# Kernel tuning notes

Hardware: AMD Instinct MI355X
Metric: run time of the kernel (lower is better)

## Reference

```python
import jax, jax.numpy as jnp
import numpy as np
from jax import lax

B, T, D, H, K = 8, 2048, 512, 4, 11
DK = D // H
LPAD = (K - 1) // 2  # sanm_shfit = 0
RPAD = K - 1 - LPAD


def setup_inputs() -> dict:
    key = jax.random.key(0)
    ks = jax.random.split(key, 7)
    x = jax.random.normal(ks[0], (B, T, D), jnp.float32)
    # binary padding-style mask (float, multiplied in; eq(0) used for attention)
    mask = jax.random.randint(ks[1], (B, 1, T), 0, 2).astype(jnp.float32)
    Wqkv = jax.random.normal(ks[2], (D, 3 * D), jnp.float32) * 0.02
    bqkv = jnp.zeros((3 * D,), jnp.float32)
    Wout = jax.random.normal(ks[3], (D, D), jnp.float32) * 0.02
    bout = jnp.zeros((D,), jnp.float32)
    # depthwise Conv1d weight: (out_ch=D, in_ch/groups=1, K)
    fsmn_w = jax.random.normal(ks[4], (D, 1, K), jnp.float32) * 0.1
    return {"x": x, "mask": mask, "Wqkv": Wqkv, "bqkv": bqkv,
            "Wout": Wout, "bout": bout, "fsmn_w": fsmn_w}


def _fsmn(v, mask, fsmn_w):
    # v: (B,T,D), mask: (B,1,T)
    m = mask.reshape(v.shape[0], -1, 1)          # (B,T,1)
    vm = v * m
    xc = vm.transpose(0, 2, 1)                   # (B,D,T)
    xp = jnp.pad(xc, ((0, 0), (0, 0), (LPAD, RPAD)))
    conv = lax.conv_general_dilated(
        xp, fsmn_w, window_strides=(1,), padding='VALID',
        dimension_numbers=('NCH', 'OIH', 'NCH'), feature_group_count=D)
    out = conv.transpose(0, 2, 1) + vm           # residual
    return out * m                               # (B,T,D)


def reference(x, mask, Wqkv, bqkv, Wout, bout, fsmn_w):
    b, t, _ = x.shape
    qkv = x @ Wqkv + bqkv                        # (B,T,3D)
    q, k, v = jnp.split(qkv, 3, axis=-1)
    fsmn_memory = _fsmn(v, mask, fsmn_w)
    qh = q.reshape(b, t, H, DK) * (DK ** -0.5)   # (B,T,H,DK)
    kh = k.reshape(b, t, H, DK)
    vh = v.reshape(b, t, H, DK)
    scores = jnp.einsum('bqhd,bkhd->bhqk', qh, kh)   # (B,H,T,T)
    km = mask[:, None, :, :]                     # (B,1,1,T) key mask
    scores = jnp.where(km == 0, -jnp.inf, scores)
    attn = jax.nn.softmax(scores, axis=-1)
    attn = jnp.where(km == 0, 0.0, attn)
    ctx = jnp.einsum('bhqk,bkhd->bqhd', attn, vh).reshape(b, t, D)
    att_outs = ctx @ Wout + bout
    return att_outs + fsmn_memory
```

## Files before the change

### kernel.cpp

```cpp
#include <hip/hip_runtime.h>
#include <hip/hip_bf16.h>
#include <stdint.h>

#define NB 8
#define NT 2048
#define ND 512
#define NH 4
#define NDK 128
#define QKV_LD 1536
#define KW 11

typedef unsigned short u16;
typedef __attribute__((ext_vector_type(4))) float f32x4;
typedef __attribute__((ext_vector_type(16))) float f32x16;
typedef __attribute__((ext_vector_type(4))) float fv4;
typedef __attribute__((ext_vector_type(8))) short s16x8;
typedef __attribute__((ext_vector_type(4))) unsigned short u16x4;
typedef __attribute__((ext_vector_type(4))) int i32x4;

#define AS1 __attribute__((address_space(1)))
#define AS3 __attribute__((address_space(3)))

__device__ __forceinline__ u16 f2bf(float f){
  unsigned u = __float_as_uint(f);
  u += 0x7fffu + ((u >> 16) & 1u);
  return (u16)(u >> 16);
}
__device__ __forceinline__ float bf2f(u16 h){ return __uint_as_float(((unsigned)h) << 16); }
__device__ __forceinline__ unsigned pack2bf(float a, float b){
  float2 t; t.x = a; t.y = b;
  __hip_bfloat162 h = __float22bfloat162_rn(t);
  return *reinterpret_cast<unsigned*>(&h);
}

__device__ __forceinline__ void transpose_body(
    const float* __restrict__ in, u16* __restrict__ out, int R, int C,
    int bx, int by, int tid)
{
  __shared__ float tile[32][33];
  const int cb = bx * 32, rb = by * 32;
  const int tx = tid & 31, ty = tid >> 5;
  #pragma unroll
  for (int i = 0; i < 4; ++i)
    tile[ty + i*8][tx] = in[(size_t)(rb + ty + i*8) * C + cb + tx];
  __syncthreads();
  #pragma unroll
  for (int i = 0; i < 4; ++i)
    out[(size_t)(cb + ty + i*8) * R + rb + tx] = f2bf(tile[tx][ty + i*8]);
}

__global__ void prep_kernel(const float* __restrict__ x, u16* __restrict__ xb,
                            const float* __restrict__ Wqkv, u16* __restrict__ wqkvT,
                            const float* __restrict__ Wout, u16* __restrict__ woutT,
                            const float* __restrict__ mask, u16* __restrict__ idxb,
                            int* __restrict__ cntb)
{
  const int bid = blockIdx.x, tid = threadIdx.x;
  if (bid < 1024){
    const int n4 = (NB*NT*ND)/4;
    for (int i = bid*256 + tid; i < n4; i += 1024*256){
      float4 v = reinterpret_cast<const float4*>(x)[i];
      u16x4 o = { f2bf(v.x), f2bf(v.y), f2bf(v.z), f2bf(v.w) };
      reinterpret_cast<u16x4*>(xb)[i] = o;
    }
  } else if (bid < 1792){
    const int idx = bid - 1024;
    transpose_body(Wqkv, wqkvT, 512, 1536, idx % 48, idx / 48, tid);
  } else if (bid < 2048){
    const int idx = bid - 1792;
    transpose_body(Wout, woutT, 512, 512, idx % 16, idx / 16, tid);
  } else {
    const int b = bid - 2048;
    __shared__ int s[256];
    const float* mb = mask + (size_t)b * NT;
    float4 a = *reinterpret_cast<const float4*>(&mb[tid*8]);
    float4 c4 = *reinterpret_cast<const float4*>(&mb[tid*8 + 4]);
    float vals[8] = {a.x, a.y, a.z, a.w, c4.x, c4.y, c4.z, c4.w};
    int lc = 0;
    #pragma unroll
    for (int j = 0; j < 8; ++j) lc += (vals[j] != 0.f);
    s[tid] = lc; __syncthreads();
    #pragma unroll
    for (int d = 1; d < 256; d <<= 1){
      const int v = (tid >= d) ? s[tid - d] : 0;
      __syncthreads();
      s[tid] += v;
      __syncthreads();
    }
    const int excl = s[tid] - lc;
    const int total = s[255];
    u16* ib = idxb + (size_t)b * NT;
    int off = excl;
    #pragma unroll
    for (int j = 0; j < 8; ++j)
      if (vals[j] != 0.f) ib[off++] = (u16)(tid*8 + j);
    const int padded = (total + 63) & ~63;
    for (int j = total + tid; j < padded; j += 256) ib[j] = 0;
    if (tid == 0) cntb[b] = total;
  }
}

__global__ __launch_bounds__(256) void kv_compact(
    const u16* __restrict__ qkvb, const u16* __restrict__ idxb,
    const int* __restrict__ cntb, u16* __restrict__ kcb, u16* __restrict__ vtc)
{
  const int b = blockIdx.y, tile = blockIdx.x, tid = threadIdx.x;
  const int total = cntb[b];
  if (tile * 64 >= ((total + 63) & ~63)) return;
  __shared__ u16 idx64[64];
  __shared__ u16 vbuf[64 * 128];
  if (tid < 64) idx64[tid] = idxb[(size_t)b * NT + tile*64 + tid];
  __syncthreads();
  #pragma unroll
  for (int h = 0; h < 4; ++h){
    #pragma unroll
    for (int i = 0; i < 4; ++i){
      const int c = i*256 + tid, key = c >> 4, ck = c & 15;
      const int srcT = idx64[key];
      const u16* sp = qkvb + ((size_t)b*NT + srcT)*QKV_LD + ND + h*NDK + ck*8;
      u16* dp = kcb + ((size_t)(b*4+h)*NT + tile*64 + key)*NDK + ck*8;
      *reinterpret_cast<s16x8*>(dp) = *reinterpret_cast<const s16x8*>(sp);
    }
    #pragma unroll
    for (int i = 0; i < 4; ++i){
      const int c = i*256 + tid, key = c >> 4, ck = c & 15;
      const int srcT = idx64[key];
      const u16* sp = qkvb + ((size_t)b*NT + srcT)*QKV_LD + 2*ND + h*NDK + ck*8;
      *reinterpret_cast<s16x8*>(&vbuf[key*128 + ck*8]) =
          *reinterpret_cast<const s16x8*>(sp);
    }
    __syncthreads();
    u16* vt = vtc + ((size_t)(b*4+h)*32 + tile) * 8192;
    #pragma unroll
    for (int i = 0; i < 4; ++i){
      const int c = i*256 + tid, kg = c >> 7, dk = c & 127;
      s16x8 ov;
      #pragma unroll
      for (int e = 0; e < 8; ++e) ov[e] = (short)vbuf[(kg*8 + e)*128 + dk];
      *reinterpret_cast<s16x8*>(&vt[c*8]) = ov;
    }
    __syncthreads();
  }
}

template<int EPI>
__global__ __launch_bounds__(256, 2) void gemm_bt(
    const u16* __restrict__ A, const u16* __restrict__ Bt, const float* __restrict__ bias,
    u16* __restrict__ Cb, float* __restrict__ Cf,
    const u16* __restrict__ qkvb, const float* __restrict__ mask,
    const float* __restrict__ fsmn_w,
    int M, int N, int Kd)
{
  __shared__ u16 As[128 * 64];
  __shared__ u16 Bs[128 * 64];
  const int tid = threadIdx.x;
  const int m0 = blockIdx.y * 128, n0 = blockIdx.x * 128;
  const int w = tid >> 6, l = tid & 63, wr = w >> 1, wc = w & 1;
  const int r15 = l & 15, g = l >> 4;

  f32x4 acc[4][4] = {};

  const int r0 = tid >> 3;
  const int scol8 = ((tid & 7) ^ (r0 & 7)) << 3;
  const u16* Ag = A  + (size_t)(m0 + r0) * Kd + scol8;
  const u16* Bg = Bt + (size_t)(n0 + r0) * Kd + scol8;
  u16* Al = &As[(size_t)tid * 8];
  u16* Bl = &Bs[(size_t)tid * 8];

  for (int k0 = 0; k0 < Kd; k0 += 64){
    #pragma unroll
    for (int i = 0; i < 4; ++i)
      __builtin_amdgcn_global_load_lds((AS1 void*)(Ag + (size_t)(i*32) * Kd + k0),
                                       (AS3 void*)(Al + i*2048), 16, 0, 0);
    #pragma unroll
    for (int i = 0; i < 4; ++i)
      __builtin_amdgcn_global_load_lds((AS1 void*)(Bg + (size_t)(i*32) * Kd + k0),
                                       (AS3 void*)(Bl + i*2048), 16, 0, 0);
    __syncthreads();
    #pragma unroll
    for (int kk = 0; kk < 2; ++kk){
      s16x8 af[4], bfr[4];
      #pragma unroll
      for (int m = 0; m < 4; ++m){
        const int R = wr*64 + m*16 + r15;
        af[m] = *reinterpret_cast<const s16x8*>(
            &As[R*64 + (((kk*4 + g) ^ (r15 & 7)) << 3)]);
      }
      #pragma unroll
      for (int n = 0; n < 4; ++n){
        const int R = wc*64 + n*16 + r15;
        bfr[n] = *reinterpret_cast<const s16x8*>(
            &Bs[R*64 + (((kk*4 + g) ^ (r15 & 7)) << 3)]);
      }
      #pragma unroll
      for (int m = 0; m < 4; ++m){
        #pragma unroll
        for (int n = 0; n < 4; ++n)
          acc[m][n] = __builtin_amdgcn_mfma_f32_16x16x32_bf16(af[m], bfr[n], acc[m][n], 0, 0, 0);
      }
    }
    __syncthreads();
  }

  if (EPI == 0){
    #pragma unroll
    for (int m = 0; m < 4; ++m){
      const int gr0 = m0 + wr*64 + m*16 + g*4;
      #pragma unroll
      for (int n = 0; n < 4; ++n){
        const int gc = n0 + wc*64 + n*16 + r15;
        const float bv = bias[gc];
        #pragma unroll
        for (int j = 0; j < 4; ++j)
          Cb[(size_t)(gr0 + j) * N + gc] = f2bf(acc[m][n][j] + bv);
      }
    }
  } else {
    float wv[4][KW];
    #pragma unroll
    for (int n = 0; n < 4; ++n){
      const int gc = n0 + wc*64 + n*16 + r15;
      #pragma unroll
      for (int i = 0; i < KW; ++i) wv[n][i] = fsmn_w[gc*KW + i];
    }
    #pragma unroll
    for (int m = 0; m < 4; ++m){
      const int gr0 = m0 + wr*64 + m*16 + g*4;
      const int bb = gr0 >> 11, t0 = gr0 & 2047;
      const float* mb = mask + (size_t)bb * NT;
      float mk[14];
      #pragma unroll
      for (int i = 0; i < 14; ++i){
        const int tau = t0 - 5 + i;
        mk[i] = ((unsigned)tau < (unsigned)NT) ? mb[tau] : 0.f;
      }
      #pragma unroll
      for (int n = 0; n < 4; ++n){
        const int gc = n0 + wc*64 + n*16 + r15;
        const float bv = bias[gc];
        const u16* vb = qkvb + (size_t)bb * NT * QKV_LD + 2*ND + gc;
        float vmv[14];
        #pragma unroll
        for (int i = 0; i < 14; ++i){
          const ptrdiff_t tau = t0 - 5 + i;
          vmv[i] = mk[i] * bf2f(vb[tau * QKV_LD]);
        }
        #pragma unroll
        for (int j = 0; j < 4; ++j){
          float conv = vmv[5 + j];
          #pragma unroll
          for (int i = 0; i < KW; ++i) conv = fmaf(wv[n][i], vmv[j + i], conv);
          Cf[(size_t)(gr0 + j) * N + gc] = acc[m][n][j] + bv + mk[5 + j] * conv;
        }
      }
    }
  }
}

#define ATT_MFMA(a, bb, c) __builtin_amdgcn_mfma_f32_32x32x16_bf16(a, bb, c, 0, 0, 0)
#define C1F 0.12751741567f

__global__ __launch_bounds__(256, 2) void attn_kernel(
    const u16* __restrict__ qkvb, const u16* __restrict__ kcb,
    const u16* __restrict__ vtc, const int* __restrict__ cntb,
    u16* __restrict__ ctxb)
{
  __shared__ u16 Ks[2][64 * 128];
  __shared__ u16 Vs[2][8 * 128 * 8];
  const int tid = threadIdx.x;
  const int w = tid >> 6, l = tid & 63, l31 = l & 31, hi = l >> 5;

  const int lin = blockIdx.x + blockIdx.y * 8;
  const int xcd = lin & 7, jj = lin >> 3;
  const int bh = xcd * 4 + (jj & 3), qblk = jj >> 2;
  const int b = bh >> 2, h = bh & 3;
  const int q0 = qblk * 128;

  const u16* qptr = qkvb + (size_t)b * NT * QKV_LD + h * NDK;
  const u16* kb   = kcb + (size_t)bh * NT * NDK;
  const u16* vtb  = vtc + (size_t)bh * 32 * 8192;
  const int total = cntb[b];
  const int ntiles = (total + 63) >> 6;

  s16x8 qf[8];
  {
    const u16* qrow = qptr + (size_t)(q0 + w*32 + l31) * QKV_LD;
    #pragma unroll
    for (int s = 0; s < 8; ++s)
      qf[s] = *reinterpret_cast<const s16x8*>(qrow + s*16 + hi*8);
  }

  float mrun = -1e30f, lrun = 0.f;
  f32x16 o0 = {}, o1 = {}, o2 = {}, o3 = {};

#define STAGE(buf, kvo) do { \
    _Pragma("unroll") \
    for (int i_ = 0; i_ < 4; ++i_){ \
      const int n_ = i_*256 + tid, kr_ = n_ >> 4, c_ = n_ & 15; \
      const u16* gp_ = kb + (size_t)((kvo) + kr_) * NDK + ((c_ ^ (kr_ & 7)) << 3); \
      __builtin_amdgcn_global_load_lds((AS1 void*)gp_, (AS3 void*)&Ks[buf][n_*8], 16, 0, 0); \
    } \
    const u16* vsrc_ = vtb + ((kvo) >> 6) * 8192; \
    _Pragma("unroll") \
    for (int i_ = 0; i_ < 4; ++i_){ \
      const int n_ = i_*256 + tid; \
      __builtin_amdgcn_global_load_lds((AS1 void*)(vsrc_ + n_*8), \
                                       (AS3 void*)&Vs[buf][n_*8], 16, 0, 0); \
    } \
  } while(0)

  if (ntiles > 0) STAGE(0, 0);
  __syncthreads();
  int cur = 0;

  for (int t = 0; t < ntiles; ++t){
    const int kv0 = t * 64;
    if (t + 1 < ntiles) STAGE(cur ^ 1, kv0 + 64);

    f32x16 d0 = {}, d1 = {};
    __builtin_amdgcn_s_setprio(1);
    #pragma unroll
    for (int s = 0; s < 8; ++s){
      const int cg = s*2 + hi;
      s16x8 kf0 = *reinterpret_cast<const s16x8*>(
          &Ks[cur][ l31*128      + ((cg ^ (l31 & 7)) << 3) ]);
      s16x8 kf1 = *reinterpret_cast<const s16x8*>(
          &Ks[cur][ (32+l31)*128 + ((cg ^ (l31 & 7)) << 3) ]);
      d0 = ATT_MFMA(kf0, qf[s], d0);
      d1 = ATT_MFMA(kf1, qf[s], d1);
    }
    __builtin_amdgcn_s_setprio(0);

    float mx0 = fmaxf(d0[0], d0[1]), mx1 = fmaxf(d0[2], d0[3]);
    float mx2 = fmaxf(d1[0], d1[1]), mx3 = fmaxf(d1[2], d1[3]);
    #pragma unroll
    for (int r = 4; r < 16; r += 4){
      mx0 = fmaxf(mx0, fmaxf(d0[r],   d0[r+1]));
      mx1 = fmaxf(mx1, fmaxf(d0[r+2], d0[r+3]));
      mx2 = fmaxf(mx2, fmaxf(d1[r],   d1[r+1]));
      mx3 = fmaxf(mx3, fmaxf(d1[r+2], d1[r+3]));
    }
    float tmx = fmaxf(fmaxf(mx0, mx1), fmaxf(mx2, mx3));
    tmx = fmaxf(tmx, __shfl_xor(tmx, 32));

    if (!__all(tmx <= mrun + 64.f)){
      const float mn = fmaxf(mrun, tmx);
      const float corr = __builtin_amdgcn_exp2f((mrun - mn) * C1F);
      mrun = mn; lrun *= corr;
      #pragma unroll
      for (int r = 0; r < 16; ++r){
        const int qs = (r & 3) + 8*(r >> 2) + 4*hi;
        const float cq = __shfl(corr, qs);
        o0[r] *= cq; o1[r] *= cq; o2[r] *= cq; o3[r] *= cq;
      }
    }

    const float mm = mrun * C1F;
    float ts = 0.f;
    if (t + 1 < ntiles){
      #pragma unroll
      for (int r = 0; r < 16; ++r){
        const float p0 = __builtin_amdgcn_exp2f(fmaf(d0[r], C1F, -mm));
        const float p1 = __builtin_amdgcn_exp2f(fmaf(d1[r], C1F, -mm));
        d0[r] = p0; d1[r] = p1; ts += p0 + p1;
      }
    } else {
      #pragma unroll
      for (int r = 0; r < 16; ++r){
        const int kidx = kv0 + (r >> 2)*8 + 4*hi + (r & 3);
        const float p0 = (kidx      < total) ? __builtin_amdgcn_exp2f(fmaf(d0[r], C1F, -mm)) : 0.f;
        const float p1 = (kidx + 32 < total) ? __builtin_amdgcn_exp2f(fmaf(d1[r], C1F, -mm)) : 0.f;
        d0[r] = p0; d1[r] = p1; ts += p0 + p1;
      }
    }
    ts += __shfl_xor(ts, 32);
    lrun += ts;

    unsigned pku[2][4][2];
    #pragma unroll
    for (int r8 = 0; r8 < 4; ++r8){
      pku[0][r8][0] = pack2bf(d0[4*r8+0], d0[4*r8+1]);
      pku[0][r8][1] = pack2bf(d0[4*r8+2], d0[4*r8+3]);
      pku[1][r8][0] = pack2bf(d1[4*r8+0], d1[4*r8+1]);
      pku[1][r8][1] = pack2bf(d1[4*r8+2], d1[4*r8+3]);
    }

    const int vb0 = hi*1024 + l31*8;
    #pragma unroll
    for (int ks = 0; ks < 4; ++ks){
      const int bb = ks >> 1, rlo = (ks & 1) * 2;
      int u0 = (int)pku[bb][rlo][0],   u1 = (int)pku[bb][rlo][1];
      int v0 = (int)pku[bb][rlo+1][0], v1 = (int)pku[bb][rlo+1][1];
      asm("v_permlane32_swap_b32 %0, %1" : "+v"(u0), "+v"(v0));
      asm("v_permlane32_swap_b32 %0, %1" : "+v"(u1), "+v"(v1));
      union { i32x4 i; s16x8 hv; } pu;
      pu.i[0] = u0; pu.i[1] = u1; pu.i[2] = v0; pu.i[3] = v1;
      const int off = ks*2048 + vb0;
      s16x8 vf0 = *reinterpret_cast<const s16x8*>(&Vs[cur][ off       ]);
      s16x8 vf1 = *reinterpret_cast<const s16x8*>(&Vs[cur][ off + 256 ]);
      s16x8 vf2 = *reinterpret_cast<const s16x8*>(&Vs[cur][ off + 512 ]);
      s16x8 vf3 = *reinterpret_cast<const s16x8*>(&Vs[cur][ off + 768 ]);
      __builtin_amdgcn_s_setprio(1);
      o0 = ATT_MFMA(pu.hv, vf0, o0);
      o1 = ATT_MFMA(pu.hv, vf1, o1);
      o2 = ATT_MFMA(pu.hv, vf2, o2);
      o3 = ATT_MFMA(pu.hv, vf3, o3);
      __builtin_amdgcn_s_setprio(0);
    }

    __syncthreads();
    cur ^= 1;
  }

  #pragma unroll
  for (int r = 0; r < 16; ++r){
    const int qs = (r & 3) + 8*(r >> 2) + 4*hi;
    const float lr = __shfl(lrun, qs);
    const float rl = (lr > 0.f) ? (1.f / lr) : 0.f;
    const int row = q0 + w*32 + qs;
    u16* cp = ctxb + (size_t)(b*NT + row) * ND + h*NDK + l31;
    cp[0]  = f2bf(o0[r] * rl);
    cp[32] = f2bf(o1[r] * rl);
    cp[64] = f2bf(o2[r] * rl);
    cp[96] = f2bf(o3[r] * rl);
  }
#undef STAGE
}

extern "C" void kernel_launch(void* const* d_in, const int* in_sizes, int n_in,
                              void* d_out, int out_size, void* d_ws, size_t ws_size,
                              hipStream_t stream) {
  const float* x      = (const float*)d_in[0];
  const float* mask   = (const float*)d_in[1];
  const float* Wqkv   = (const float*)d_in[2];
  const float* bqkv   = (const float*)d_in[3];
  const float* Wout   = (const float*)d_in[4];
  const float* bout   = (const float*)d_in[5];
  const float* fsmn_w = (const float*)d_in[6];
  float* out = (float*)d_out;

  char* ws = (char*)d_ws;
  u16* xb    = (u16*)ws;
  u16* kcb   = (u16*)ws;
  u16* wqkvT = (u16*)(ws + 16777216);
  u16* woutT = (u16*)(ws + 18350080);
  u16* qkvb  = (u16*)(ws + 18874368);
  u16* ctxb  = (u16*)(ws + 69206016);
  u16* vtc   = (u16*)(ws + 85983232);
  u16* idxb  = (u16*)(ws + 102760448);
  int* cntb  = (int*)(ws + 102793216);

  prep_kernel<<<2056, 256, 0, stream>>>(x, xb, Wqkv, wqkvT, Wout, woutT,
                                        mask, idxb, cntb);
  gemm_bt<0><<<dim3(1536/128, 16384/128), 256, 0, stream>>>(
      xb, wqkvT, bqkv, qkvb, nullptr, nullptr, nullptr, nullptr, NB*NT, QKV_LD, ND);
  kv_compact<<<dim3(32, 8), 256, 0, stream>>>(qkvb, idxb, cntb, kcb, vtc);
  attn_kernel<<<dim3(8, 64), 256, 0, stream>>>(qkvb, kcb, vtc, cntb, ctxb);
  gemm_bt<1><<<dim3(512/128, 16384/128), 256, 0, stream>>>(
      ctxb, woutT, bout, nullptr, out, qkvb, mask, fsmn_w, NB*NT, ND, ND);
}
```

Before: 129.2 us.

## Compute K/V projection only for unmasked rows and write compacted layouts directly

Splits the QKV GEMM into a Q GEMM and a K/V GEMM. The K/V GEMM gathers only the unmasked token rows of x and writes K and transposed V directly in the compacted attention layouts, which removes the separate kv_compact kernel and the K/V projection work for masked tokens. The FSMN epilogue in the output GEMM now reads V from the compacted transposed buffer through a new position map built in prep, in place of the full qkv buffer. This adds gather indirection and scattered stores in the K/V epilogue.

```diff
diff --git a/kernel.cpp b/kernel.cpp
--- a/kernel.cpp
+++ b/kernel.cpp
@@ -7,7 +7,6 @@
 #define ND 512
 #define NH 4
 #define NDK 128
-#define QKV_LD 1536
 #define KW 11
 
 typedef unsigned short u16;
@@ -53,7 +52,7 @@
                             const float* __restrict__ Wqkv, u16* __restrict__ wqkvT,
                             const float* __restrict__ Wout, u16* __restrict__ woutT,
                             const float* __restrict__ mask, u16* __restrict__ idxb,
-                            int* __restrict__ cntb)
+                            u16* __restrict__ pos16, int* __restrict__ cntb)
 {
   const int bid = blockIdx.x, tid = threadIdx.x;
   if (bid < 1024){
@@ -90,66 +89,23 @@
     const int excl = s[tid] - lc;
     const int total = s[255];
     u16* ib = idxb + (size_t)b * NT;
+    u16* pb = pos16 + (size_t)b * NT;
     int off = excl;
     #pragma unroll
-    for (int j = 0; j < 8; ++j)
-      if (vals[j] != 0.f) ib[off++] = (u16)(tid*8 + j);
-    const int padded = (total + 63) & ~63;
+    for (int j = 0; j < 8; ++j){
+      const int t = tid*8 + j;
+      if (vals[j] != 0.f){ ib[off] = (u16)t; pb[t] = (u16)off; ++off; }
+      else pb[t] = (u16)0xFFFF;
+    }
+    const int padded = (total + 127) & ~127;
     for (int j = total + tid; j < padded; j += 256) ib[j] = 0;
     if (tid == 0) cntb[b] = total;
   }
 }
 
-__global__ __launch_bounds__(256) void kv_compact(
-    const u16* __restrict__ qkvb, const u16* __restrict__ idxb,
-    const int* __restrict__ cntb, u16* __restrict__ kcb, u16* __restrict__ vtc)
-{
-  const int b = blockIdx.y, tile = blockIdx.x, tid = threadIdx.x;
-  const int total = cntb[b];
-  if (tile * 64 >= ((total + 63) & ~63)) return;
-  __shared__ u16 idx64[64];
-  __shared__ u16 vbuf[64 * 128];
-  if (tid < 64) idx64[tid] = idxb[(size_t)b * NT + tile*64 + tid];
-  __syncthreads();
-  #pragma unroll
-  for (int h = 0; h < 4; ++h){
-    #pragma unroll
-    for (int i = 0; i < 4; ++i){
-      const int c = i*256 + tid, key = c >> 4, ck = c & 15;
-      const int srcT = idx64[key];
-      const u16* sp = qkvb + ((size_t)b*NT + srcT)*QKV_LD + ND + h*NDK + ck*8;
-      u16* dp = kcb + ((size_t)(b*4+h)*NT + tile*64 + key)*NDK + ck*8;
-      *reinterpret_cast<s16x8*>(dp) = *reinterpret_cast<const s16x8*>(sp);
-    }
-    #pragma unroll
-    for (int i = 0; i < 4; ++i){
-      const int c = i*256 + tid, key = c >> 4, ck = c & 15;
-      const int srcT = idx64[key];
-      const u16* sp = qkvb + ((size_t)b*NT + srcT)*QKV_LD + 2*ND + h*NDK + ck*8;
-      *reinterpret_cast<s16x8*>(&vbuf[key*128 + ck*8]) =
-          *reinterpret_cast<const s16x8*>(sp);
-    }
-    __syncthreads();
-    u16* vt = vtc + ((size_t)(b*4+h)*32 + tile) * 8192;
-    #pragma unroll
-    for (int i = 0; i < 4; ++i){
-      const int c = i*256 + tid, kg = c >> 7, dk = c & 127;
-      s16x8 ov;
-      #pragma unroll
-      for (int e = 0; e < 8; ++e) ov[e] = (short)vbuf[(kg*8 + e)*128 + dk];
-      *reinterpret_cast<s16x8*>(&vt[c*8]) = ov;
-    }
-    __syncthreads();
-  }
-}
-
-template<int EPI>
-__global__ __launch_bounds__(256, 2) void gemm_bt(
+__global__ __launch_bounds__(256, 2) void gemm_q(
     const u16* __restrict__ A, const u16* __restrict__ Bt, const float* __restrict__ bias,
-    u16* __restrict__ Cb, float* __restrict__ Cf,
-    const u16* __restrict__ qkvb, const float* __restrict__ mask,
-    const float* __restrict__ fsmn_w,
-    int M, int N, int Kd)
+    u16* __restrict__ Cb, int M, int N, int Kd)
 {
   __shared__ u16 As[128 * 64];
   __shared__ u16 Bs[128 * 64];
@@ -183,14 +139,12 @@
       #pragma unroll
       for (int m = 0; m < 4; ++m){
         const int R = wr*64 + m*16 + r15;
-        af[m] = *reinterpret_cast<const s16x8*>(
-            &As[R*64 + (((kk*4 + g) ^ (r15 & 7)) << 3)]);
+        af[m] = *reinterpret_cast<const s16x8*>(&As[R*64 + (((kk*4 + g) ^ (r15 & 7)) << 3)]);
       }
       #pragma unroll
       for (int n = 0; n < 4; ++n){
         const int R = wc*64 + n*16 + r15;
-        bfr[n] = *reinterpret_cast<const s16x8*>(
-            &Bs[R*64 + (((kk*4 + g) ^ (r15 & 7)) << 3)]);
+        bfr[n] = *reinterpret_cast<const s16x8*>(&Bs[R*64 + (((kk*4 + g) ^ (r15 & 7)) << 3)]);
       }
       #pragma unroll
       for (int m = 0; m < 4; ++m){
@@ -202,56 +156,202 @@
     __syncthreads();
   }
 
-  if (EPI == 0){
-    #pragma unroll
-    for (int m = 0; m < 4; ++m){
-      const int gr0 = m0 + wr*64 + m*16 + g*4;
-      #pragma unroll
-      for (int n = 0; n < 4; ++n){
-        const int gc = n0 + wc*64 + n*16 + r15;
-        const float bv = bias[gc];
-        #pragma unroll
-        for (int j = 0; j < 4; ++j)
-          Cb[(size_t)(gr0 + j) * N + gc] = f2bf(acc[m][n][j] + bv);
-      }
-    }
-  } else {
-    float wv[4][KW];
+  #pragma unroll
+  for (int m = 0; m < 4; ++m){
+    const int gr0 = m0 + wr*64 + m*16 + g*4;
     #pragma unroll
     for (int n = 0; n < 4; ++n){
       const int gc = n0 + wc*64 + n*16 + r15;
-      #pragma unroll
-      for (int i = 0; i < KW; ++i) wv[n][i] = fsmn_w[gc*KW + i];
-    }
-    #pragma unroll
-    for (int m = 0; m < 4; ++m){
-      const int gr0 = m0 + wr*64 + m*16 + g*4;
-      const int bb = gr0 >> 11, t0 = gr0 & 2047;
-      const float* mb = mask + (size_t)bb * NT;
-      float mk[14];
+      const float bv = bias[gc];
+      #pragma unroll
+      for (int j = 0; j < 4; ++j)
+        Cb[(size_t)(gr0 + j) * N + gc] = f2bf(acc[m][n][j] + bv);
+    }
+  }
+}
+
+__global__ __launch_bounds__(256, 2) void gemm_kv(
+    const u16* __restrict__ xb, const u16* __restrict__ Bt, const float* __restrict__ bias,
+    const u16* __restrict__ idxb, const int* __restrict__ cntb,
+    u16* __restrict__ kcb, u16* __restrict__ vtc)
+{
+  const int b = blockIdx.y >> 4, mb = blockIdx.y & 15;
+  const int total = cntb[b];
+  const int padded = (total + 127) & ~127;
+  const int m0 = mb * 128;
+  if (m0 >= padded) return;
+  const int Kd = ND, n0 = blockIdx.x * 128;
+
+  __shared__ u16 As[128 * 64];
+  __shared__ u16 Bs[128 * 64];
+  const int tid = threadIdx.x;
+  const int w = tid >> 6, l = tid & 63, wr = w >> 1, wc = w & 1;
+  const int r15 = l & 15, g = l >> 4;
+
+  f32x4 acc[4][4] = {};
+
+  const int r0 = tid >> 3;
+  const int scol8 = ((tid & 7) ^ (r0 & 7)) << 3;
+  const u16* ib = idxb + (size_t)b * NT;
+  const u16* Ab = xb + (size_t)b * NT * ND;
+  const u16* Ag0 = Ab + (size_t)ib[m0 + r0      ] * Kd + scol8;
+  const u16* Ag1 = Ab + (size_t)ib[m0 + r0 + 32 ] * Kd + scol8;
+  const u16* Ag2 = Ab + (size_t)ib[m0 + r0 + 64 ] * Kd + scol8;
+  const u16* Ag3 = Ab + (size_t)ib[m0 + r0 + 96 ] * Kd + scol8;
+  const u16* Bg = Bt + (size_t)(n0 + r0) * Kd + scol8;
+  u16* Al = &As[(size_t)tid * 8];
+  u16* Bl = &Bs[(size_t)tid * 8];
+
+  for (int k0 = 0; k0 < Kd; k0 += 64){
+    __builtin_amdgcn_global_load_lds((AS1 void*)(Ag0 + k0), (AS3 void*)(Al        ), 16, 0, 0);
+    __builtin_amdgcn_global_load_lds((AS1 void*)(Ag1 + k0), (AS3 void*)(Al + 2048 ), 16, 0, 0);
+    __builtin_amdgcn_global_load_lds((AS1 void*)(Ag2 + k0), (AS3 void*)(Al + 4096 ), 16, 0, 0);
+    __builtin_amdgcn_global_load_lds((AS1 void*)(Ag3 + k0), (AS3 void*)(Al + 6144 ), 16, 0, 0);
+    #pragma unroll
+    for (int i = 0; i < 4; ++i)
+      __builtin_amdgcn_global_load_lds((AS1 void*)(Bg + (size_t)(i*32) * Kd + k0),
+                                       (AS3 void*)(Bl + i*2048), 16, 0, 0);
+    __syncthreads();
+    #pragma unroll
+    for (int kk = 0; kk < 2; ++kk){
+      s16x8 af[4], bfr[4];
+      #pragma unroll
+      for (int m = 0; m < 4; ++m){
+        const int R = wr*64 + m*16 + r15;
+        af[m] = *reinterpret_cast<const s16x8*>(&As[R*64 + (((kk*4 + g) ^ (r15 & 7)) << 3)]);
+      }
+      #pragma unroll
+      for (int n = 0; n < 4; ++n){
+        const int R = wc*64 + n*16 + r15;
+        bfr[n] = *reinterpret_cast<const s16x8*>(&Bs[R*64 + (((kk*4 + g) ^ (r15 & 7)) << 3)]);
+      }
+      #pragma unroll
+      for (int m = 0; m < 4; ++m){
+        #pragma unroll
+        for (int n = 0; n < 4; ++n)
+          acc[m][n] = __builtin_amdgcn_mfma_f32_16x16x32_bf16(af[m], bfr[n], acc[m][n], 0, 0, 0);
+      }
+    }
+    __syncthreads();
+  }
+
+  const bool isK = (n0 < 512);
+  #pragma unroll
+  for (int m = 0; m < 4; ++m){
+    const int gr0 = m0 + wr*64 + m*16 + g*4;
+    #pragma unroll
+    for (int n = 0; n < 4; ++n){
+      const int gc = n0 + wc*64 + n*16 + r15;
+      const float bv = bias[gc];
+      const int d = isK ? gc : (gc - 512);
+      const int bh = b*4 + (d >> 7), dk = d & 127;
+      #pragma unroll
+      for (int j = 0; j < 4; ++j){
+        const u16 hv = f2bf(acc[m][n][j] + bv);
+        const int pos = gr0 + j;
+        if (isK){
+          kcb[((size_t)bh*NT + pos)*NDK + dk] = hv;
+        } else {
+          vtc[((size_t)bh*32 + (pos >> 6))*8192 + ((pos & 63) >> 3)*1024 + dk*8 + (pos & 7)] = hv;
+        }
+      }
+    }
+  }
+}
+
+__global__ __launch_bounds__(256, 2) void gemm_out(
+    const u16* __restrict__ A, const u16* __restrict__ Bt, const float* __restrict__ bias,
+    float* __restrict__ Cf, const u16* __restrict__ pos16, const u16* __restrict__ vtc,
+    const float* __restrict__ fsmn_w, int M, int N, int Kd)
+{
+  __shared__ u16 As[128 * 64];
+  __shared__ u16 Bs[128 * 64];
+  const int tid = threadIdx.x;
+  const int m0 = blockIdx.y * 128, n0 = blockIdx.x * 128;
+  const int w = tid >> 6, l = tid & 63, wr = w >> 1, wc = w & 1;
+  const int r15 = l & 15, g = l >> 4;
+
+  f32x4 acc[4][4] = {};
+
+  const int r0 = tid >> 3;
+  const int scol8 = ((tid & 7) ^ (r0 & 7)) << 3;
+  const u16* Ag = A  + (size_t)(m0 + r0) * Kd + scol8;
+  const u16* Bg = Bt + (size_t)(n0 + r0) * Kd + scol8;
+  u16* Al = &As[(size_t)tid * 8];
+  u16* Bl = &Bs[(size_t)tid * 8];
+
+  for (int k0 = 0; k0 < Kd; k0 += 64){
+    #pragma unroll
+    for (int i = 0; i < 4; ++i)
+      __builtin_amdgcn_global_load_lds((AS1 void*)(Ag + (size_t)(i*32) * Kd + k0),
+                                       (AS3 void*)(Al + i*2048), 16, 0, 0);
+    #pragma unroll
+    for (int i = 0; i < 4; ++i)
+      __builtin_amdgcn_global_load_lds((AS1 void*)(Bg + (size_t)(i*32) * Kd + k0),
+                                       (AS3 void*)(Bl + i*2048), 16, 0, 0);
+    __syncthreads();
+    #pragma unroll
+    for (int kk = 0; kk < 2; ++kk){
+      s16x8 af[4], bfr[4];
+      #pragma unroll
+      for (int m = 0; m < 4; ++m){
+        const int R = wr*64 + m*16 + r15;
+        af[m] = *reinterpret_cast<const s16x8*>(&As[R*64 + (((kk*4 + g) ^ (r15 & 7)) << 3)]);
+      }
+      #pragma unroll
+      for (int n = 0; n < 4; ++n){
+        const int R = wc*64 + n*16 + r15;
+        bfr[n] = *reinterpret_cast<const s16x8*>(&Bs[R*64 + (((kk*4 + g) ^ (r15 & 7)) << 3)]);
+      }
+      #pragma unroll
+      for (int m = 0; m < 4; ++m){
+        #pragma unroll
+        for (int n = 0; n < 4; ++n)
+          acc[m][n] = __builtin_amdgcn_mfma_f32_16x16x32_bf16(af[m], bfr[n], acc[m][n], 0, 0, 0);
+      }
+    }
+    __syncthreads();
+  }
+
+  float wv[4][KW];
+  #pragma unroll
+  for (int n = 0; n < 4; ++n){
+    const int gc = n0 + wc*64 + n*16 + r15;
+    #pragma unroll
+    for (int i = 0; i < KW; ++i) wv[n][i] = fsmn_w[gc*KW + i];
+  }
+  #pragma unroll
+  for (int m = 0; m < 4; ++m){
+    const int gr0 = m0 + wr*64 + m*16 + g*4;
+    const int bb = gr0 >> 11, t0 = gr0 & 2047;
+    const u16* pb = pos16 + (size_t)bb * NT;
+    int tap[14];
+    #pragma unroll
+    for (int i = 0; i < 14; ++i){
+      const int tau = t0 - 5 + i;
+      tap[i] = ((unsigned)tau < (unsigned)NT) ? (int)pb[tau] : 0xFFFF;
+    }
+    #pragma unroll
+    for (int n = 0; n < 4; ++n){
+      const int gc = n0 + wc*64 + n*16 + r15;
+      const float bv = bias[gc];
+      const int hh = gc >> 7, dk = gc & 127;
+      const u16* vtb = vtc + ((size_t)(bb*4 + hh)*32)*8192 + dk*8;
+      float vmv[14];
       #pragma unroll
       for (int i = 0; i < 14; ++i){
-        const int tau = t0 - 5 + i;
-        mk[i] = ((unsigned)tau < (unsigned)NT) ? mb[tau] : 0.f;
-      }
-      #pragma unroll
-      for (int n = 0; n < 4; ++n){
-        const int gc = n0 + wc*64 + n*16 + r15;
-        const float bv = bias[gc];
-        const u16* vb = qkvb + (size_t)bb * NT * QKV_LD + 2*ND + gc;
-        float vmv[14];
+        const int p = tap[i];
+        const int pc = (p == 0xFFFF) ? 0 : p;
+        const float v = bf2f(vtb[(pc >> 6)*8192 + ((pc & 63) >> 3)*1024 + (pc & 7)]);
+        vmv[i] = (p == 0xFFFF) ? 0.f : v;
+      }
+      #pragma unroll
+      for (int j = 0; j < 4; ++j){
+        float conv = vmv[5 + j];
         #pragma unroll
-        for (int i = 0; i < 14; ++i){
-          const ptrdiff_t tau = t0 - 5 + i;
-          vmv[i] = mk[i] * bf2f(vb[tau * QKV_LD]);
-        }
-        #pragma unroll
-        for (int j = 0; j < 4; ++j){
-          float conv = vmv[5 + j];
-          #pragma unroll
-          for (int i = 0; i < KW; ++i) conv = fmaf(wv[n][i], vmv[j + i], conv);
-          Cf[(size_t)(gr0 + j) * N + gc] = acc[m][n][j] + bv + mk[5 + j] * conv;
-        }
+        for (int i = 0; i < KW; ++i) conv = fmaf(wv[n][i], vmv[j + i], conv);
+        const float fs = (tap[5 + j] != 0xFFFF) ? conv : 0.f;
+        Cf[(size_t)(gr0 + j) * N + gc] = acc[m][n][j] + bv + fs;
       }
     }
   }
@@ -261,7 +361,7 @@
 #define C1F 0.12751741567f
 
 __global__ __launch_bounds__(256, 2) void attn_kernel(
-    const u16* __restrict__ qkvb, const u16* __restrict__ kcb,
+    const u16* __restrict__ qb, const u16* __restrict__ kcb,
     const u16* __restrict__ vtc, const int* __restrict__ cntb,
     u16* __restrict__ ctxb)
 {
@@ -276,7 +376,6 @@
   const int b = bh >> 2, h = bh & 3;
   const int q0 = qblk * 128;
 
-  const u16* qptr = qkvb + (size_t)b * NT * QKV_LD + h * NDK;
   const u16* kb   = kcb + (size_t)bh * NT * NDK;
   const u16* vtb  = vtc + (size_t)bh * 32 * 8192;
   const int total = cntb[b];
@@ -284,7 +383,7 @@
 
   s16x8 qf[8];
   {
-    const u16* qrow = qptr + (size_t)(q0 + w*32 + l31) * QKV_LD;
+    const u16* qrow = qb + (size_t)(b*NT + q0 + w*32 + l31) * ND + h * NDK;
     #pragma unroll
     for (int s = 0; s < 8; ++s)
       qf[s] = *reinterpret_cast<const s16x8*>(qrow + s*16 + hi*8);
@@ -441,21 +540,23 @@
 
   char* ws = (char*)d_ws;
   u16* xb    = (u16*)ws;
-  u16* kcb   = (u16*)ws;
   u16* wqkvT = (u16*)(ws + 16777216);
   u16* woutT = (u16*)(ws + 18350080);
-  u16* qkvb  = (u16*)(ws + 18874368);
+  u16* qb    = (u16*)(ws + 18874368);
+  u16* kcb   = (u16*)(ws + 35651584);
+  u16* vtc   = (u16*)(ws + 52428800);
   u16* ctxb  = (u16*)(ws + 69206016);
-  u16* vtc   = (u16*)(ws + 85983232);
-  u16* idxb  = (u16*)(ws + 102760448);
-  int* cntb  = (int*)(ws + 102793216);
+  u16* idxb  = (u16*)(ws + 85983232);
+  u16* pos16 = (u16*)(ws + 86016000);
+  int* cntb  = (int*)(ws + 86048768);
 
   prep_kernel<<<2056, 256, 0, stream>>>(x, xb, Wqkv, wqkvT, Wout, woutT,
-                                        mask, idxb, cntb);
-  gemm_bt<0><<<dim3(1536/128, 16384/128), 256, 0, stream>>>(
-      xb, wqkvT, bqkv, qkvb, nullptr, nullptr, nullptr, nullptr, NB*NT, QKV_LD, ND);
-  kv_compact<<<dim3(32, 8), 256, 0, stream>>>(qkvb, idxb, cntb, kcb, vtc);
-  attn_kernel<<<dim3(8, 64), 256, 0, stream>>>(qkvb, kcb, vtc, cntb, ctxb);
-  gemm_bt<1><<<dim3(512/128, 16384/128), 256, 0, stream>>>(
-      ctxb, woutT, bout, nullptr, out, qkvb, mask, fsmn_w, NB*NT, ND, ND);
-}
+                                        mask, idxb, pos16, cntb);
+  gemm_q<<<dim3(512/128, 16384/128), 256, 0, stream>>>(
+      xb, wqkvT, bqkv, qb, NB*NT, ND, ND);
+  gemm_kv<<<dim3(1024/128, 128), 256, 0, stream>>>(
+      xb, wqkvT + 512*512, bqkv + 512, idxb, cntb, kcb, vtc);
+  attn_kernel<<<dim3(8, 64), 256, 0, stream>>>(qb, kcb, vtc, cntb, ctxb);
+  gemm_out<<<dim3(512/128, 16384/128), 256, 0, stream>>>(
+      ctxb, woutT, bout, out, pos16, vtc, fsmn_w, NB*NT, ND, ND);
+}
```

Measured after the change: 153.2 us. 1.19x slower.
